# Optimization experiments

Hardware: AMD Instinct MI355X
Metric: run time of the kernel (lower is better)

Reference implementation:

```python
import jax, jax.numpy as jnp
import numpy as np

N, FIN, FOUT = 4096, 512, 256
ALPHA = 0.2          # LeakyReLU negative slope
NEG_INF = -9e15      # mask value from the torch source


def setup_inputs() -> dict:
    key = jax.random.key(0)
    ks = jax.random.split(key, 11)
    h = jax.random.normal(ks[0], (N, FIN), dtype=jnp.float32)
    adj_n = jax.random.randint(ks[1], (N, N), 0, 2, dtype=jnp.int32)
    adj_d = jax.random.randint(ks[2], (N, N), 0, 2, dtype=jnp.int32)
    G_nd = jax.random.normal(ks[3], (2, N, FOUT), dtype=jnp.float32)
    # learned parameters (xavier-ish scale)
    W_n = jax.random.normal(ks[4], (FIN, FOUT), dtype=jnp.float32) * 0.05
    a1_n = jax.random.normal(ks[5], (FOUT, 1), dtype=jnp.float32) * 0.05
    a2_n = jax.random.normal(ks[6], (FOUT, 1), dtype=jnp.float32) * 0.05
    W_d = jax.random.normal(ks[7], (FIN, FOUT), dtype=jnp.float32) * 0.05
    a1_d = jax.random.normal(ks[8], (FOUT, 1), dtype=jnp.float32) * 0.05
    a2_d = jax.random.normal(ks[9], (FOUT, 1), dtype=jnp.float32) * 0.05
    scale = jnp.zeros((1,), dtype=jnp.float32)
    return {"h": h, "adj_n": adj_n, "adj_d": adj_d, "G_nd": G_nd,
            "W_n": W_n, "a1_n": a1_n, "a2_n": a2_n,
            "W_d": W_d, "a1_d": a1_d, "a2_d": a2_d, "scale": scale}


def _gat(h, adj, W, a1, a2):
    # Wh: [N, FOUT]
    Wh = h @ W
    # outer-sum attention logits: e[i,j] = leakyrelu(Wh_i.a1 + Wh_j.a2)
    e = jax.nn.leaky_relu((Wh @ a1) + (Wh @ a2).T, negative_slope=ALPHA)  # [N, N]
    att = jnp.where(adj > 0, e, jnp.float32(NEG_INF))
    att = jax.nn.softmax(att, axis=-1)
    # dropout is identity in eval mode
    return jax.nn.elu(att @ Wh)  # [N, FOUT]


def reference(h, adj_n, adj_d, G_nd, W_n, a1_n, a2_n, W_d, a1_d, a2_d, scale):
    f_n_S = _gat(h, adj_n, W_n, a1_n, a2_n)
    f_d_S = _gat(h, adj_d, W_d, a1_d, a2_d)
    # The G_nd cross-attention branch (f_nd_C) in the torch source is computed
    # but never used in the returned value; omitted here (jit would DCE it).
    return f_n_S + f_d_S
```

## Files before the change

### kernel.cpp

```cpp
#include <hip/hip_runtime.h>

#define N_NODES 4096
#define FIN     512
#define FOUT    256

typedef __attribute__((ext_vector_type(8))) short bf16x8s;
typedef __attribute__((ext_vector_type(4))) float f32x4;
typedef __attribute__((ext_vector_type(4))) int   i32x4;
typedef __attribute__((ext_vector_type(8))) unsigned short u16x8;
typedef unsigned short u16;
typedef unsigned int   u32;

__device__ inline u16 f2b(float f) {
    union { float f; unsigned int u; } v; v.f = f;
    unsigned int r = v.u + 0x7fffu + ((v.u >> 16) & 1u);
    return (u16)(r >> 16);
}

__global__ __launch_bounds__(256) void prep_kernel(
    const float* __restrict__ h, const float* __restrict__ Wn,
    const float* __restrict__ Wd,
    u16* __restrict__ hb, u16* __restrict__ WTb, float* __restrict__ s12)
{
    __shared__ u16 tl[64 * 72];
    const int t = threadIdx.x;
    const int bid = blockIdx.x;

    if (bid < 1024) {
        int idx = (bid * 256 + t) * 8;
        float4 f0 = *(const float4*)&h[idx];
        float4 f1 = *(const float4*)&h[idx + 4];
        u16x8 o;
        o[0]=f2b(f0.x); o[1]=f2b(f0.y); o[2]=f2b(f0.z); o[3]=f2b(f0.w);
        o[4]=f2b(f1.x); o[5]=f2b(f1.y); o[6]=f2b(f1.z); o[7]=f2b(f1.w);
        *(u16x8*)&hb[idx] = o;
    } else if (bid < 1088) {
        int id = bid - 1024;
        int kx = id & 7, ny = (id >> 3) & 3, b = id >> 5;
        const float* W = b ? Wd : Wn;
        int k0 = kx * 64, n0 = ny * 64;
        int kr = t >> 2, nc0 = (t & 3) * 16;
        const float* src = W + (size_t)(k0 + kr) * FOUT + n0 + nc0;
        #pragma unroll
        for (int jv = 0; jv < 4; ++jv) {
            float4 f = *(const float4*)(src + jv * 4);
            tl[(nc0 + jv * 4 + 0) * 72 + kr] = f2b(f.x);
            tl[(nc0 + jv * 4 + 1) * 72 + kr] = f2b(f.y);
            tl[(nc0 + jv * 4 + 2) * 72 + kr] = f2b(f.z);
            tl[(nc0 + jv * 4 + 3) * 72 + kr] = f2b(f.w);
        }
        __syncthreads();
        int n = t >> 2, kc0 = (t & 3) * 16;
        u16* dst = WTb + ((size_t)b << 17) + (size_t)(n0 + n) * FIN + k0 + kc0;
        *(uint4*)dst       = *(uint4*)&tl[n * 72 + kc0];
        *(uint4*)(dst + 8) = *(uint4*)&tl[n * 72 + kc0 + 8];
    } else {
        float4 z = {0.f, 0.f, 0.f, 0.f};
        float4* p4 = (float4*)s12;
        #pragma unroll
        for (int k = 0; k < 16; ++k) p4[k * 256 + t] = z;
    }
}

__global__ __launch_bounds__(256) void wh_gemm_kernel(
    const u16* __restrict__ hb, const u16* __restrict__ WTb,
    const float* __restrict__ a1n, const float* __restrict__ a2n,
    const float* __restrict__ a1d, const float* __restrict__ a2d,
    u16* __restrict__ WhT, float* __restrict__ s1, float* __restrict__ s2)
{
    __shared__ u16 smem[8192];
    u16* a_lds = smem;
    u16* b_lds = smem + 4096;

    const int t = threadIdx.x, lane = t & 63, w = t >> 6;
    const int q = lane >> 4, ln = lane & 15;
    const int i0 = blockIdx.x * 64, n0 = blockIdx.y * 64, b = blockIdx.z;
    const u16* wt = WTb + ((size_t)b << 17);

    f32x4 acc[4];
    #pragma unroll
    for (int i = 0; i < 4; ++i) acc[i] = (f32x4){0.f, 0.f, 0.f, 0.f};

    for (int kt = 0; kt < 8; ++kt) {
        const int k0 = kt * 64;
        __syncthreads();
        #pragma unroll
        for (int it = 0; it < 2; ++it) {
            int chunk = it * 256 + t;
            int r = chunk >> 3, kc = chunk & 7;
            const u16* g = hb + (size_t)(i0 + r) * FIN + k0 + ((kc ^ (r & 7)) * 8);
            u16* l = a_lds + (it * 256 + w * 64) * 8;
            __builtin_amdgcn_global_load_lds(
                (const __attribute__((address_space(1))) void*)g,
                (__attribute__((address_space(3))) void*)l, 16, 0, 0);
        }
        #pragma unroll
        for (int it = 0; it < 2; ++it) {
            int chunk = it * 256 + t;
            int n = chunk >> 3, kc = chunk & 7;
            const u16* g = wt + (size_t)(n0 + n) * FIN + k0 + ((kc ^ (n & 7)) * 8);
            u16* l = b_lds + (it * 256 + w * 64) * 8;
            __builtin_amdgcn_global_load_lds(
                (const __attribute__((address_space(1))) void*)g,
                (__attribute__((address_space(3))) void*)l, 16, 0, 0);
        }
        __syncthreads();
        #pragma unroll
        for (int ks = 0; ks < 2; ++ks) {
            int sw = ((ks * 4 + q) ^ (ln & 7)) * 8;
            bf16x8s af = *(const bf16x8s*)&a_lds[(w * 16 + ln) * 64 + sw];
            #pragma unroll
            for (int nt = 0; nt < 4; ++nt) {
                bf16x8s bfv = *(const bf16x8s*)&b_lds[(nt * 16 + ln) * 64 + sw];
                acc[nt] = __builtin_amdgcn_mfma_f32_16x16x32_bf16(af, bfv, acc[nt], 0, 0, 0);
            }
        }
    }

    {
        const float* a1 = b ? a1d : a1n;
        const float* a2 = b ? a2d : a2n;
        float s1p[4] = {0.f, 0.f, 0.f, 0.f};
        float s2p[4] = {0.f, 0.f, 0.f, 0.f};
        #pragma unroll
        for (int nt = 0; nt < 4; ++nt) {
            float va1 = a1[n0 + nt * 16 + ln];
            float va2 = a2[n0 + nt * 16 + ln];
            #pragma unroll
            for (int r = 0; r < 4; ++r) {
                s1p[r] += acc[nt][r] * va1;
                s2p[r] += acc[nt][r] * va2;
            }
        }
        #pragma unroll
        for (int r = 0; r < 4; ++r) {
            #pragma unroll
            for (int off = 8; off >= 1; off >>= 1) {
                s1p[r] += __shfl_xor(s1p[r], off);
                s2p[r] += __shfl_xor(s2p[r], off);
            }
            if (ln == 0) {
                int row = i0 + w * 16 + q * 4 + r;
                atomicAdd(&s1[b * N_NODES + row], s1p[r]);
                atomicAdd(&s2[b * N_NODES + row], s2p[r]);
            }
        }
    }

    __syncthreads();
    #pragma unroll
    for (int nt = 0; nt < 4; ++nt)
        #pragma unroll
        for (int r = 0; r < 4; ++r)
            smem[(nt * 16 + ln) * 72 + (w * 16 + q * 4 + r)] = f2b(acc[nt][r]);
    __syncthreads();
    {
        const int nl = t >> 2, is = (t & 3) * 16;
        u16* dst = WhT + ((size_t)b << 20) + (size_t)(n0 + nl) * N_NODES + i0 + is;
        *(uint4*)dst       = *(uint4*)&smem[nl * 72 + is];
        *(uint4*)(dst + 8) = *(uint4*)&smem[nl * 72 + is + 8];
    }
}

__global__ __launch_bounds__(256) void attn_kernel(
    const int* __restrict__ adj_n, const int* __restrict__ adj_d,
    const u16* __restrict__ WhT,
    const float* __restrict__ s1, const float* __restrict__ s2,
    float* __restrict__ num_ws, float* __restrict__ den_ws, int nsplit)
{
    __shared__ u16 wht_lds[16384];
    __shared__ u16 p_lds[8192];

    const int t = threadIdx.x, lane = t & 63, w = t >> 6;
    const int q = lane >> 4, ln = lane & 15;
    const int b = blockIdx.z, split = blockIdx.y;
    const int i0 = blockIdx.x * 128;
    const int jcount = N_NODES / nsplit;
    const int ntiles = jcount / 64;

    const int* adjb = b ? adj_d : adj_n;
    const u16* whtB = WhT + ((size_t)b << 20);
    const float* s1b = s1 + b * N_NODES;
    const float* s2b = s2 + b * N_NODES;

    const int pr = t >> 3;
    const int cw = t & 7;
    const int pc = cw * 8;
    float  s1v[4];
    size_t arow[4];
    #pragma unroll
    for (int r = 0; r < 4; ++r) {
        s1v[r]  = s1b[i0 + pr + 32 * r];
        arow[r] = (size_t)(i0 + pr + 32 * r) * N_NODES + pc;
    }

    float den[4] = {0.f, 0.f, 0.f, 0.f};

    f32x4 acc[8][4];
    #pragma unroll
    for (int mt = 0; mt < 8; ++mt)
        #pragma unroll
        for (int nt = 0; nt < 4; ++nt) acc[mt][nt] = (f32x4){0.f, 0.f, 0.f, 0.f};

    const int jbase = split * jcount;
    i32x4 apf[4][2];
    #pragma unroll
    for (int r = 0; r < 4; ++r) {
        apf[r][0] = __builtin_nontemporal_load((const i32x4*)&adjb[arow[r] + jbase]);
        apf[r][1] = __builtin_nontemporal_load((const i32x4*)&adjb[arow[r] + jbase + 4]);
    }
    float4 sv0_pf = *(const float4*)&s2b[jbase + pc];
    float4 sv1_pf = *(const float4*)&s2b[jbase + pc + 4];

    for (int jt = 0; jt < ntiles; ++jt) {
        const int j0 = jbase + jt * 64;
        __syncthreads();
        #pragma unroll
        for (int it = 0; it < 8; ++it) {
            int chunk = it * 256 + t;
            int n = chunk >> 3, kc = chunk & 7;
            const u16* g = whtB + (size_t)n * N_NODES + j0 + ((kc ^ (n & 7)) * 8);
            u16* l = wht_lds + (it * 256 + w * 64) * 8;
            __builtin_amdgcn_global_load_lds(
                (const __attribute__((address_space(1))) void*)g,
                (__attribute__((address_space(3))) void*)l, 16, 0, 0);
        }
        float svf[8] = {sv0_pf.x, sv0_pf.y, sv0_pf.z, sv0_pf.w,
                        sv1_pf.x, sv1_pf.y, sv1_pf.z, sv1_pf.w};
        const int swp = ((cw ^ (pr & 7)) * 8);
        #pragma unroll
        for (int r = 0; r < 4; ++r) {
            int v[8] = {apf[r][0][0], apf[r][0][1], apf[r][0][2], apf[r][0][3],
                        apf[r][1][0], apf[r][1][1], apf[r][1][2], apf[r][1][3]};
            u16x8 pk;
            #pragma unroll
            for (int jj = 0; jj < 8; ++jj) {
                float x = s1v[r] + svf[jj];
                float p = (v[jj] > 0) ? __expf(fmaxf(x, 0.2f * x)) : 0.f;
                den[r] += p;
                pk[jj] = f2b(p);
            }
            *(u16x8*)&p_lds[(pr + 32 * r) * 64 + swp] = pk;
        }
        __syncthreads();
        if (jt + 1 < ntiles) {
            const int jn = j0 + 64;
            #pragma unroll
            for (int r = 0; r < 4; ++r) {
                apf[r][0] = __builtin_nontemporal_load((const i32x4*)&adjb[arow[r] + jn]);
                apf[r][1] = __builtin_nontemporal_load((const i32x4*)&adjb[arow[r] + jn + 4]);
            }
            sv0_pf = *(const float4*)&s2b[jn + pc];
            sv1_pf = *(const float4*)&s2b[jn + pc + 4];
        }
        #pragma unroll
        for (int ks = 0; ks < 2; ++ks) {
            int sw = ((ks * 4 + q) ^ (ln & 7)) * 8;
            #pragma unroll
            for (int nt = 0; nt < 4; ++nt) {
                bf16x8s bfv = *(const bf16x8s*)&wht_lds[(w * 64 + nt * 16 + ln) * 64 + sw];
                #pragma unroll
                for (int mt = 0; mt < 8; ++mt) {
                    bf16x8s af = *(const bf16x8s*)&p_lds[(mt * 16 + ln) * 64 + sw];
                    acc[mt][nt] = __builtin_amdgcn_mfma_f32_16x16x32_bf16(af, bfv, acc[mt][nt], 0, 0, 0);
                }
            }
        }
    }
    #pragma unroll
    for (int r = 0; r < 4; ++r) {
        den[r] += __shfl_down(den[r], 4, 8);
        den[r] += __shfl_down(den[r], 2, 8);
        den[r] += __shfl_down(den[r], 1, 8);
    }
    const size_t pbase = (size_t)(b * nsplit + split) * N_NODES;
    if ((t & 7) == 0) {
        #pragma unroll
        for (int r = 0; r < 4; ++r)
            den_ws[pbase + i0 + pr + 32 * r] = den[r];
    }
    #pragma unroll
    for (int mt = 0; mt < 8; ++mt)
        #pragma unroll
        for (int r = 0; r < 4; ++r) {
            int row = mt * 16 + q * 4 + r;
            #pragma unroll
            for (int nt = 0; nt < 4; ++nt)
                __builtin_nontemporal_store(acc[mt][nt][r],
                    &num_ws[(pbase + i0 + row) * FOUT + w * 64 + nt * 16 + ln]);
        }
}

__global__ __launch_bounds__(256) void reduce_kernel(
    const float* __restrict__ num_ws, const float* __restrict__ den_ws,
    float* __restrict__ out, int nsplit)
{
    int gid = blockIdx.x * 256 + threadIdx.x;
    int i = gid >> 6;
    int f4 = (gid & 63) * 4;
    float4 o = {0.f, 0.f, 0.f, 0.f};
    #pragma unroll
    for (int b = 0; b < 2; ++b) {
        float4 num = {0.f, 0.f, 0.f, 0.f};
        float den = 0.f;
        for (int s = 0; s < nsplit; ++s) {
            f32x4 v = __builtin_nontemporal_load(
                (const f32x4*)&num_ws[((size_t)(b * nsplit + s) * N_NODES + i) * FOUT + f4]);
            num.x += v[0]; num.y += v[1]; num.z += v[2]; num.w += v[3];
            den += den_ws[(size_t)(b * nsplit + s) * N_NODES + i];
        }
        float inv = 1.0f / den;
        float e0 = num.x * inv, e1 = num.y * inv, e2 = num.z * inv, e3 = num.w * inv;
        o.x += (e0 > 0.f) ? e0 : expm1f(e0);
        o.y += (e1 > 0.f) ? e1 : expm1f(e1);
        o.z += (e2 > 0.f) ? e2 : expm1f(e2);
        o.w += (e3 > 0.f) ? e3 : expm1f(e3);
    }
    *(float4*)&out[(size_t)i * FOUT + f4] = o;
}

extern "C" void kernel_launch(void* const* d_in, const int* in_sizes, int n_in,
                              void* d_out, int out_size, void* d_ws, size_t ws_size,
                              hipStream_t stream) {
    const float* h    = (const float*)d_in[0];
    const int*   adjn = (const int*)d_in[1];
    const int*   adjd = (const int*)d_in[2];
    const float* Wn   = (const float*)d_in[4];
    const float* a1n  = (const float*)d_in[5];
    const float* a2n  = (const float*)d_in[6];
    const float* Wd   = (const float*)d_in[7];
    const float* a1d  = (const float*)d_in[8];
    const float* a2d  = (const float*)d_in[9];

    char* ws = (char*)d_ws;
    u16*  WhT  = (u16*)ws;
    float* s1  = (float*)(ws + ((size_t)8 << 20));
    float* s2  = s1 + 2 * N_NODES;
    float* den = s2 + 2 * N_NODES;
    size_t num_off = ((size_t)8 << 20) + ((size_t)400 << 10);
    u16*  hb   = (u16*)(ws + num_off);
    u16*  WTb  = (u16*)(ws + num_off + ((size_t)4 << 20));
    float* num = (float*)(ws + num_off);

    const size_t per_split = (size_t)2 * N_NODES * FOUT * sizeof(float);
    int nsplit = (ws_size >= num_off + 8 * per_split) ? 8 : 4;

    prep_kernel<<<1089, 256, 0, stream>>>(h, Wn, Wd, hb, WTb, s1);
    wh_gemm_kernel<<<dim3(64, 4, 2), 256, 0, stream>>>(hb, WTb, a1n, a2n, a1d, a2d, WhT, s1, s2);
    attn_kernel<<<dim3(32, nsplit, 2), 256, 0, stream>>>(adjn, adjd, WhT, s1, s2, num, den, nsplit);
    reduce_kernel<<<1024, 256, 0, stream>>>(num, den, (float*)d_out, nsplit);
}
```

Baseline: 224.7 us.

## Double-buffer WhT tile in LDS and prefetch next tile after MFMA

Doubles the LDS buffer for the WhT tile so the next tile's global-to-LDS load is issued after the current tile's MFMA work, overlapping with the next iteration's probability computation. The MFMA inner loop is also regrouped to hold four A fragments in registers and reuse each B fragment across them, cutting repeated LDS reads of P. It adds a second barrier per iteration and doubles WhT LDS use, which may lower occupancy.

```diff
diff --git a/kernel.cpp b/kernel.cpp
--- a/kernel.cpp
+++ b/kernel.cpp
@@ -168,7 +168,7 @@
     const float* __restrict__ s1, const float* __restrict__ s2,
     float* __restrict__ num_ws, float* __restrict__ den_ws, int nsplit)
 {
-    __shared__ u16 wht_lds[16384];
+    __shared__ u16 wht_lds[2][16384];
     __shared__ u16 p_lds[8192];
 
     const int t = threadIdx.x, lane = t & 63, w = t >> 6;
@@ -203,6 +203,19 @@
         for (int nt = 0; nt < 4; ++nt) acc[mt][nt] = (f32x4){0.f, 0.f, 0.f, 0.f};
 
     const int jbase = split * jcount;
+
+    {
+        #pragma unroll
+        for (int it = 0; it < 8; ++it) {
+            int chunk = it * 256 + t;
+            int n = chunk >> 3, kc = chunk & 7;
+            const u16* g = whtB + (size_t)n * N_NODES + jbase + ((kc ^ (n & 7)) * 8);
+            u16* l = &wht_lds[0][(it * 256 + w * 64) * 8];
+            __builtin_amdgcn_global_load_lds(
+                (const __attribute__((address_space(1))) void*)g,
+                (__attribute__((address_space(3))) void*)l, 16, 0, 0);
+        }
+    }
     i32x4 apf[4][2];
     #pragma unroll
     for (int r = 0; r < 4; ++r) {
@@ -213,18 +226,7 @@
     float4 sv1_pf = *(const float4*)&s2b[jbase + pc + 4];
 
     for (int jt = 0; jt < ntiles; ++jt) {
-        const int j0 = jbase + jt * 64;
-        __syncthreads();
-        #pragma unroll
-        for (int it = 0; it < 8; ++it) {
-            int chunk = it * 256 + t;
-            int n = chunk >> 3, kc = chunk & 7;
-            const u16* g = whtB + (size_t)n * N_NODES + j0 + ((kc ^ (n & 7)) * 8);
-            u16* l = wht_lds + (it * 256 + w * 64) * 8;
-            __builtin_amdgcn_global_load_lds(
-                (const __attribute__((address_space(1))) void*)g,
-                (__attribute__((address_space(3))) void*)l, 16, 0, 0);
-        }
+        const int cur = jt & 1;
         float svf[8] = {sv0_pf.x, sv0_pf.y, sv0_pf.z, sv0_pf.w,
                         sv1_pf.x, sv1_pf.y, sv1_pf.z, sv1_pf.w};
         const int swp = ((cw ^ (pr & 7)) * 8);
@@ -243,8 +245,39 @@
             *(u16x8*)&p_lds[(pr + 32 * r) * 64 + swp] = pk;
         }
         __syncthreads();
+        const u16* wbuf = wht_lds[cur];
+        #pragma unroll
+        for (int ks = 0; ks < 2; ++ks) {
+            int sw = ((ks * 4 + q) ^ (ln & 7)) * 8;
+            #pragma unroll
+            for (int mg = 0; mg < 2; ++mg) {
+                bf16x8s af[4];
+                #pragma unroll
+                for (int m2 = 0; m2 < 4; ++m2)
+                    af[m2] = *(const bf16x8s*)&p_lds[((mg * 4 + m2) * 16 + ln) * 64 + sw];
+                #pragma unroll
+                for (int nt = 0; nt < 4; ++nt) {
+                    bf16x8s bfv = *(const bf16x8s*)&wbuf[(w * 64 + nt * 16 + ln) * 64 + sw];
+                    #pragma unroll
+                    for (int m2 = 0; m2 < 4; ++m2)
+                        acc[mg * 4 + m2][nt] = __builtin_amdgcn_mfma_f32_16x16x32_bf16(
+                            af[m2], bfv, acc[mg * 4 + m2][nt], 0, 0, 0);
+                }
+            }
+        }
+        __syncthreads();
         if (jt + 1 < ntiles) {
-            const int jn = j0 + 64;
+            const int jn = jbase + (jt + 1) * 64;
+            #pragma unroll
+            for (int it = 0; it < 8; ++it) {
+                int chunk = it * 256 + t;
+                int n = chunk >> 3, kc = chunk & 7;
+                const u16* g = whtB + (size_t)n * N_NODES + jn + ((kc ^ (n & 7)) * 8);
+                u16* l = &wht_lds[cur ^ 1][(it * 256 + w * 64) * 8];
+                __builtin_amdgcn_global_load_lds(
+                    (const __attribute__((address_space(1))) void*)g,
+                    (__attribute__((address_space(3))) void*)l, 16, 0, 0);
+            }
             #pragma unroll
             for (int r = 0; r < 4; ++r) {
                 apf[r][0] = __builtin_nontemporal_load((const i32x4*)&adjb[arow[r] + jn]);
@@ -252,19 +285,6 @@
             }
             sv0_pf = *(const float4*)&s2b[jn + pc];
             sv1_pf = *(const float4*)&s2b[jn + pc + 4];
-        }
-        #pragma unroll
-        for (int ks = 0; ks < 2; ++ks) {
-            int sw = ((ks * 4 + q) ^ (ln & 7)) * 8;
-            #pragma unroll
-            for (int nt = 0; nt < 4; ++nt) {
-                bf16x8s bfv = *(const bf16x8s*)&wht_lds[(w * 64 + nt * 16 + ln) * 64 + sw];
-                #pragma unroll
-                for (int mt = 0; mt < 8; ++mt) {
-                    bf16x8s af = *(const bf16x8s*)&p_lds[(mt * 16 + ln) * 64 + sw];
-                    acc[mt][nt] = __builtin_amdgcn_mfma_f32_16x16x32_bf16(af, bfv, acc[mt][nt], 0, 0, 0);
-                }
-            }
         }
     }
     #pragma unroll
```

After: 227.5 us. No clear change (+1.2%).
